# Optimization experiments

Measured on AMD Instinct MI355X. Metric: run time of the kernel, lower is better.

## Reference

```python
import jax, jax.numpy as jnp
import numpy as np


def _interp_bilinear_ac(x, out_h, out_w):
    """Bilinear resize with align_corners=True, NCHW."""
    n, c, h, w = x.shape
    ys = jnp.linspace(0.0, h - 1.0, out_h)
    xs = jnp.linspace(0.0, w - 1.0, out_w)
    y0 = jnp.floor(ys).astype(jnp.int32)
    y1 = jnp.minimum(y0 + 1, h - 1)
    wy = (ys - y0.astype(x.dtype))[None, None, :, None]
    x0 = jnp.floor(xs).astype(jnp.int32)
    x1 = jnp.minimum(x0 + 1, w - 1)
    wx = (xs - x0.astype(x.dtype))[None, None, None, :]
    # interpolate along H then W
    xh = x[:, :, y0, :] * (1.0 - wy) + x[:, :, y1, :] * wy  # [n,c,out_h,w]
    out = xh[:, :, :, x0] * (1.0 - wx) + xh[:, :, :, x1] * wx  # [n,c,out_h,out_w]
    return out


def setup_inputs() -> dict:
    key = jax.random.key(0)
    ks = jax.random.split(key, 7)
    return {
        "aspp": jax.random.normal(ks[0], (8, 128, 32, 32), jnp.float32),
        "f3": jax.random.normal(ks[1], (8, 128, 32, 32), jnp.float32),
        "inp": jax.random.normal(ks[2], (8, 4, 512, 512), jnp.float32),
        "cam": jax.random.normal(ks[3], (8, 21, 64, 64), jnp.float32),
        "w_aspp": jax.random.normal(ks[4], (64, 128), jnp.float32) * 0.05,
        "w_f3": jax.random.normal(ks[5], (64, 128), jnp.float32) * 0.05,
        "w_f9": jax.random.normal(ks[6], (128, 132), jnp.float32) * 0.05,
    }


def reference(aspp, f3, inp, cam, w_aspp, w_f3, w_f9):
    n, c, h, w = cam.shape
    # 1x1 convs (no bias) as channel matmuls
    f3p = jnp.einsum('oc,nchw->nohw', w_f3, f3)
    asppp = jnp.einsum('oc,nchw->nohw', w_aspp, aspp)
    # bilinear upsample (align_corners=True) to cam resolution
    asppp = _interp_bilinear_ac(asppp, h, w)
    x_s = _interp_bilinear_ac(inp, h, w)
    f3p = _interp_bilinear_ac(f3p, h, w)
    f = jnp.concatenate([x_s, asppp, f3p], axis=1)  # [n,132,h,w]
    f = jnp.einsum('oc,nchw->nohw', w_f9, f)        # [n,128,h,w]
    f = f.reshape(n, -1, h * w)                     # [n,128,hw]
    f = f / (jnp.linalg.norm(f, axis=1, keepdims=True) + 1e-5)
    # affinity: [n, hw, hw]
    aff = jax.nn.relu(jnp.einsum('ncp,ncq->npq', f, f))
    aff = aff / (jnp.sum(aff, axis=1, keepdims=True) + 1e-5)
    cam_rv = jnp.matmul(cam.reshape(n, -1, h * w), aff).reshape(n, -1, h, w)
    return cam_rv
```

## Files before the change

kernel.cpp:

```cpp
#include <hip/hip_runtime.h>
#include <math.h>

typedef unsigned short u16;
typedef unsigned int u32;
typedef __attribute__((ext_vector_type(8))) short bf16x8;
typedef __attribute__((ext_vector_type(4))) short short4v;
typedef __attribute__((ext_vector_type(4))) float f32x4;
typedef __attribute__((ext_vector_type(16))) float f32x16;

#define HW32 1024
#define HW64 4096
#define KCAM 21
#define PB 64
#define PSPLIT 4
#define FT_STR 168

static __device__ __forceinline__ u16 f2bf(float x) {
  u32 u = __float_as_uint(x);
  u32 r = (u + 0x7FFFu + ((u >> 16) & 1u)) >> 16;
  return (u16)r;
}
static __device__ __forceinline__ float bf2f(u16 h) {
  return __uint_as_float(((u32)h) << 16);
}

__global__ __launch_bounds__(256) void k_conv32(
    const float* __restrict__ aspp, const float* __restrict__ f3,
    const float* __restrict__ w_aspp, const float* __restrict__ w_f3,
    const float* __restrict__ w_f9,
    float* __restrict__ a32, float* __restrict__ g32,
    u16* __restrict__ whi, u16* __restrict__ wlo)
{
  const int pt = blockIdx.x, which = blockIdx.y >> 2, jq = blockIdx.y & 3,
            n = blockIdx.z;

  if (blockIdx.y == 0) {
    const int bid = blockIdx.z * 4 + blockIdx.x;
#pragma unroll
    for (int k = 0; k < 3; ++k) {
      const int idx = bid * 256 + threadIdx.x + k * 8192;
      if (idx < 128 * 160) {
        const int o = idx / 160, c = idx - o * 160;
        const float v = (c < 132) ? w_f9[o * 132 + c] : 0.f;
        const u16 h = f2bf(v);
        whi[idx] = h;
        wlo[idx] = f2bf(v - bf2f(h));
      }
    }
  }

  const float* x = (which == 0 ? aspp : f3) + (size_t)n * 128 * HW32;
  const float* w = (which == 0 ? w_aspp : w_f3) + jq * 16 * 128;
  float* out = (which == 0 ? a32 : g32) + (size_t)n * 64 * HW32 + (size_t)jq * 16 * HW32;

  __shared__ __align__(16) float wlds[16 * 128];
  for (int i = threadIdx.x; i < 16 * 128; i += 256) wlds[i] = w[i];
  __syncthreads();

  const int p = pt * 256 + threadIdx.x;
  float acc[16];
#pragma unroll
  for (int j = 0; j < 16; ++j) acc[j] = 0.f;

  for (int c0 = 0; c0 < 128; c0 += 8) {
    float xv[8];
#pragma unroll
    for (int cc = 0; cc < 8; ++cc) xv[cc] = x[(size_t)(c0 + cc) * HW32 + p];
#pragma unroll
    for (int j = 0; j < 16; ++j) {
      const float4 w0 = *reinterpret_cast<const float4*>(&wlds[j * 128 + c0]);
      const float4 w1 = *reinterpret_cast<const float4*>(&wlds[j * 128 + c0 + 4]);
      acc[j] = fmaf(w0.x, xv[0], acc[j]);
      acc[j] = fmaf(w0.y, xv[1], acc[j]);
      acc[j] = fmaf(w0.z, xv[2], acc[j]);
      acc[j] = fmaf(w0.w, xv[3], acc[j]);
      acc[j] = fmaf(w1.x, xv[4], acc[j]);
      acc[j] = fmaf(w1.y, xv[5], acc[j]);
      acc[j] = fmaf(w1.z, xv[6], acc[j]);
      acc[j] = fmaf(w1.w, xv[7], acc[j]);
    }
  }
  for (int j = 0; j < 16; ++j) out[(size_t)j * HW32 + p] = acc[j];
}

__global__ __launch_bounds__(256) void k_build_f(
    const float* __restrict__ inp, const float* __restrict__ a32,
    const float* __restrict__ g32, const u16* __restrict__ whi,
    const u16* __restrict__ wlo, const float* __restrict__ cam,
    u16* __restrict__ fhi_g, u16* __restrict__ camA)
{
  const int y2 = blockIdx.x, n = blockIdx.y;
  const int tid = threadIdx.x;

  __shared__ __align__(16) u16 feat[128 * FT_STR];
  __shared__ __align__(16) u16 wh[128 * FT_STR];
  __shared__ __align__(16) u16 wl[128 * FT_STR];

  for (int ch = tid; ch < 2560; ch += 256) {
    const int o = ch / 20, c8 = (ch - o * 20) * 8;
    *(bf16x8*)&wh[o * FT_STR + c8] = *(const bf16x8*)(whi + o * 160 + c8);
    *(bf16x8*)&wl[o * FT_STR + c8] = *(const bf16x8*)(wlo + o * 160 + c8);
  }

  {
    u16* dst = camA + ((size_t)n * 32 + y2) * HW64;
    if (y2 < KCAM) {
      const float* src = cam + ((size_t)n * KCAM + y2) * HW64;
      for (int i = tid; i < HW64; i += 256) dst[i] = f2bf(src[i]);
    } else {
      const u16 v = (y2 == KCAM) ? f2bf(1.f) : (u16)0;
      for (int i = tid; i < HW64; i += 256) dst[i] = v;
    }
  }

  const float s512 = 511.f / 63.f, s32 = 31.f / 63.f;
  const int yA0i = y2 * 2, yA1i = y2 * 2 + 1;
  const float sA0 = yA0i * s512, sA1 = yA1i * s512;
  const int y0A0 = (int)sA0, y0A1 = (int)sA1;
  const float wyA0 = sA0 - y0A0, wyA1 = sA1 - y0A1;
  const int y1A0 = min(y0A0 + 1, 511), y1A1 = min(y0A1 + 1, 511);
  const float sB0 = yA0i * s32, sB1 = yA1i * s32;
  const int y0B0 = (int)sB0, y0B1 = (int)sB1;
  const float wyB0 = sB0 - y0B0, wyB1 = sB1 - y0B1;
  const int y1B0 = min(y0B0 + 1, 31), y1B1 = min(y0B1 + 1, 31);

  for (int idx = tid; idx < 132 * 128; idx += 256) {
    const int c = idx >> 7;
    const int pos = idx & 127;
    const int ly = pos >> 6, x = pos & 63;
    const int y0A = ly ? y0A1 : y0A0, y1A = ly ? y1A1 : y1A0;
    const float wyA = ly ? wyA1 : wyA0;
    const int y0B = ly ? y0B1 : y0B0, y1B = ly ? y1B1 : y1B0;
    const float wyB = ly ? wyB1 : wyB0;
    float v;
    if (c < 4) {
      const float sx = x * s512;
      const int x0 = (int)sx;
      const float wx = sx - (float)x0;
      const int x1 = min(x0 + 1, 511);
      const float* im = inp + (size_t)(n * 4 + c) * 512 * 512;
      const float v00 = im[y0A * 512 + x0], v01 = im[y0A * 512 + x1];
      const float v10 = im[y1A * 512 + x0], v11 = im[y1A * 512 + x1];
      v = (v00 * (1.f - wx) + v01 * wx) * (1.f - wyA) +
          (v10 * (1.f - wx) + v11 * wx) * wyA;
    } else {
      const float* im = (c < 68) ? a32 + (size_t)(n * 64 + (c - 4)) * HW32
                                 : g32 + (size_t)(n * 64 + (c - 68)) * HW32;
      const float sx = x * s32;
      const int x0 = (int)sx;
      const float wx = sx - (float)x0;
      const int x1 = min(x0 + 1, 31);
      const float v00 = im[y0B * 32 + x0], v01 = im[y0B * 32 + x1];
      const float v10 = im[y1B * 32 + x0], v11 = im[y1B * 32 + x1];
      v = (v00 * (1.f - wx) + v01 * wx) * (1.f - wyB) +
          (v10 * (1.f - wx) + v11 * wx) * wyB;
    }
    feat[pos * FT_STR + c] = f2bf(v);
  }
  for (int idx = tid; idx < 28 * 128; idx += 256) {
    const int c = 132 + (idx >> 7), pos = idx & 127;
    feat[pos * FT_STR + c] = 0;
  }
  __syncthreads();

  const int lane = tid & 63, wave = tid >> 6;
  const int l15 = lane & 15, l4 = lane >> 4;

  f32x4 acc[8][2];
#pragma unroll
  for (int m = 0; m < 8; ++m)
#pragma unroll
    for (int nf = 0; nf < 2; ++nf) acc[m][nf] = {0.f, 0.f, 0.f, 0.f};

#pragma unroll
  for (int s = 0; s < 5; ++s) {
    bf16x8 B[2];
#pragma unroll
    for (int nf = 0; nf < 2; ++nf)
      B[nf] = *(const bf16x8*)&feat[(wave * 32 + nf * 16 + l15) * FT_STR +
                                    s * 32 + l4 * 8];
#pragma unroll
    for (int m = 0; m < 8; ++m) {
      const int wo = (m * 16 + l15) * FT_STR + s * 32 + l4 * 8;
      const bf16x8 Ahi = *(const bf16x8*)&wh[wo];
      const bf16x8 Alo = *(const bf16x8*)&wl[wo];
#pragma unroll
      for (int nf = 0; nf < 2; ++nf) {
        acc[m][nf] = __builtin_amdgcn_mfma_f32_16x16x32_bf16(Ahi, B[nf], acc[m][nf], 0, 0, 0);
        acc[m][nf] = __builtin_amdgcn_mfma_f32_16x16x32_bf16(Alo, B[nf], acc[m][nf], 0, 0, 0);
      }
    }
  }

#pragma unroll
  for (int nf = 0; nf < 2; ++nf) {
    float ss = 0.f;
#pragma unroll
    for (int m = 0; m < 8; ++m)
#pragma unroll
      for (int i = 0; i < 4; ++i) ss = fmaf(acc[m][nf][i], acc[m][nf][i], ss);
    ss += __shfl_xor(ss, 16);
    ss += __shfl_xor(ss, 32);
    const float inv = 1.f / (sqrtf(ss) + 1e-5f);
    const int pos = wave * 32 + nf * 16 + l15;
    u16* fp = fhi_g + ((size_t)n * HW64 + (size_t)(y2 * 2 + (pos >> 6)) * 64 +
                       (pos & 63)) * 128 + l4 * 4;
#pragma unroll
    for (int m = 0; m < 8; ++m) {
      const float v0 = acc[m][nf][0] * inv, v1 = acc[m][nf][1] * inv;
      const float v2 = acc[m][nf][2] * inv, v3 = acc[m][nf][3] * inv;
      union { u32 d[2]; short4v h; } P;
      asm("v_cvt_pk_bf16_f32 %0, %1, %2" : "=v"(P.d[0]) : "v"(v0), "v"(v1));
      asm("v_cvt_pk_bf16_f32 %0, %1, %2" : "=v"(P.d[1]) : "v"(v2), "v"(v3));
      *(short4v*)(fp + m * 16) = P.h;
    }
  }
}

__global__ __launch_bounds__(256) void k_fused(
    const u16* __restrict__ fhi_g, const u16* __restrict__ camA,
    float* __restrict__ part)
{
  __shared__ __align__(16) u16 fh[2][PB * 128];

  const int gx = blockIdx.x;
  const int n = gx & 7;
  const int rest = gx >> 3;
  const int qt = rest & 15;
  const int ps = rest >> 4;
  const int tid = threadIdx.x;
  const int lane = tid & 63;
  const int wq = tid >> 6;
  const int l31 = lane & 31;
  const int lh = lane >> 5;
  const int qb = qt * 256;

  const u16* fbase = fhi_g + (size_t)n * HW64 * 128;

  bf16x8 Bq[2][8];
#pragma unroll
  for (int qh = 0; qh < 2; ++qh) {
    const size_t rowo = (size_t)(qb + wq * 64 + qh * 32 + l31) * 128;
#pragma unroll
    for (int ks = 0; ks < 8; ++ks)
      Bq[qh][ks] = *(const bf16x8*)(fbase + rowo + ks * 16 + lh * 8);
  }

  f32x16 nacc0, nacc1;
#pragma unroll
  for (int i = 0; i < 16; ++i) { nacc0[i] = 0.f; nacc1[i] = 0.f; }

  const int p_base = ps * (HW64 / PSPLIT);
  const int sp = tid >> 2;
  const int scb = (tid & 3) * 64;
  const int xorw = (sp & 7) << 4;
  int wofs[4];
#pragma unroll
  for (int k = 0; k < 4; ++k)
    wofs[k] = sp * 128 + (((scb + k * 16) ^ xorw) >> 1);
  const int xorr = (l31 & 7) << 4;

  {
    const u16* src = fbase + (size_t)(p_base + sp) * 128 + scb / 2;
#pragma unroll
    for (int k = 0; k < 4; ++k)
      *(bf16x8*)&fh[0][wofs[k]] = *(const bf16x8*)(src + k * 8);
  }

  int cur = 0;
  for (int t = 0; t < (HW64 / PSPLIT) / PB; ++t) {
    const int p0 = p_base + t * PB;
    __syncthreads();

    bf16x8 nxt[4];
    if (t < 15) {
      const u16* src = fbase + (size_t)(p0 + PB + sp) * 128 + scb / 2;
#pragma unroll
      for (int k = 0; k < 4; ++k) nxt[k] = *(const bf16x8*)(src + k * 8);
    }

    bf16x8 Ac[4];
#pragma unroll
    for (int kst = 0; kst < 4; ++kst) {
      union { short4v h[2]; bf16x8 v; } A;
      const u16* cp = camA + ((size_t)n * 32 + l31) * HW64 + p0 + kst * 16 + lh * 4;
      A.h[0] = *(const short4v*)cp;
      A.h[1] = *(const short4v*)(cp + 8);
      Ac[kst] = A.v;
    }

    f32x16 accS[2][2];
#pragma unroll
    for (int ks = 0; ks < 8; ++ks) {
      const int cb = (ks * 32 + (lh << 4)) ^ xorr;
      bf16x8 Ah[2];
#pragma unroll
      for (int mt = 0; mt < 2; ++mt)
        Ah[mt] = *(const bf16x8*)&fh[cur][(mt * 32 + l31) * 128 + (cb >> 1)];
      if (ks == 0) {
        f32x16 z;
#pragma unroll
        for (int i = 0; i < 16; ++i) z[i] = 0.f;
#pragma unroll
        for (int mt = 0; mt < 2; ++mt) {
          accS[mt][0] = __builtin_amdgcn_mfma_f32_32x32x16_bf16(Ah[mt], Bq[0][0], z, 0, 0, 0);
          accS[mt][1] = __builtin_amdgcn_mfma_f32_32x32x16_bf16(Ah[mt], Bq[1][0], z, 0, 0, 0);
        }
      } else {
#pragma unroll
        for (int mt = 0; mt < 2; ++mt) {
          accS[mt][0] = __builtin_amdgcn_mfma_f32_32x32x16_bf16(Ah[mt], Bq[0][ks], accS[mt][0], 0, 0, 0);
          accS[mt][1] = __builtin_amdgcn_mfma_f32_32x32x16_bf16(Ah[mt], Bq[1][ks], accS[mt][1], 0, 0, 0);
        }
      }
    }

#pragma unroll
    for (int kst = 0; kst < 4; ++kst) {
      const int mt = kst >> 1, h8 = (kst & 1) * 8;
#pragma unroll
      for (int qh = 0; qh < 2; ++qh) {
        union { u32 d[4]; bf16x8 v; } W;
#pragma unroll
        for (int i = 0; i < 4; ++i) {
          const float a0 = fmaxf(accS[mt][qh][h8 + 2 * i], 0.f);
          const float a1 = fmaxf(accS[mt][qh][h8 + 2 * i + 1], 0.f);
          asm("v_cvt_pk_bf16_f32 %0, %1, %2" : "=v"(W.d[i]) : "v"(a0), "v"(a1));
        }
        if (qh == 0)
          nacc0 = __builtin_amdgcn_mfma_f32_32x32x16_bf16(Ac[kst], W.v, nacc0, 0, 0, 0);
        else
          nacc1 = __builtin_amdgcn_mfma_f32_32x32x16_bf16(Ac[kst], W.v, nacc1, 0, 0, 0);
      }
    }

    if (t < 15) {
#pragma unroll
      for (int k = 0; k < 4; ++k) *(bf16x8*)&fh[cur ^ 1][wofs[k]] = nxt[k];
    }
    cur ^= 1;
  }

#pragma unroll
  for (int qh = 0; qh < 2; ++qh) {
    const int qg = qb + wq * 64 + qh * 32 + l31;
#pragma unroll
    for (int r = 0; r < 16; ++r) {
      const int row = (r & 3) + 8 * (r >> 2) + 4 * lh;
      if (row < 22)
        part[(((size_t)n * PSPLIT + ps) * 22 + row) * HW64 + qg] =
            (qh == 0) ? nacc0[r] : nacc1[r];
    }
  }
}

__global__ __launch_bounds__(256) void k_final(
    const float* __restrict__ part, float* __restrict__ out, int total)
{
  const int idx = blockIdx.x * 256 + threadIdx.x;
  if (idx >= total) return;
  const int n = idx / (KCAM * HW64);
  const int r = idx - n * (KCAM * HW64);
  const int k = r >> 12;
  const int q = r & 4095;
  const float* base = part + (size_t)n * PSPLIT * 22 * HW64;
  float num = 0.f, den = 0.f;
#pragma unroll
  for (int p = 0; p < PSPLIT; ++p) {
    num += base[((size_t)p * 22 + k) * HW64 + q];
    den += base[((size_t)p * 22 + 21) * HW64 + q];
  }
  out[idx] = num / (den + 1e-5f);
}

extern "C" void kernel_launch(void* const* d_in, const int* in_sizes, int n_in,
                              void* d_out, int out_size, void* d_ws, size_t ws_size,
                              hipStream_t stream) {
  const float* aspp   = (const float*)d_in[0];
  const float* f3     = (const float*)d_in[1];
  const float* inp    = (const float*)d_in[2];
  const float* cam    = (const float*)d_in[3];
  const float* w_aspp = (const float*)d_in[4];
  const float* w_f3   = (const float*)d_in[5];
  const float* w_f9   = (const float*)d_in[6];
  float* out = (float*)d_out;

  u16*   fhi  = (u16*)d_ws;
  u16*   camA = fhi + 4194304;
  u16*   whi  = camA + 1048576;
  u16*   wlo  = whi + 20480;
  float* part = (float*)(wlo + 20480);
  float* a32  = part;
  float* g32  = a32 + 524288;

  k_conv32<<<dim3(4, 8, 8), 256, 0, stream>>>(aspp, f3, w_aspp, w_f3, w_f9,
                                              a32, g32, whi, wlo);
  k_build_f<<<dim3(32, 8), 256, 0, stream>>>(inp, a32, g32, whi, wlo, cam,
                                             fhi, camA);
  k_fused<<<512, 256, 0, stream>>>(fhi, camA, part);
  k_final<<<2688, 256, 0, stream>>>(part, out, 8 * KCAM * HW64);
}
```

Baseline: 99.61 us.

## Fuse split-K reduction into main kernel via last-block atomic counter

Removes the separate k_final launch. Each k_fused block increments a per-(n,qt) counter after writing its partial sums, and the last of the PSPLIT blocks to arrive reduces the partials and writes the normalized output. This saves one kernel launch and its scheduling gap. In exchange it adds a memset launch, threadfences, and a serialized tail in which only the last block per tile does the reduction.

After: 186.8 us. 1.88x slower.

```diff
diff --git a/kernel.cpp b/kernel.cpp
--- a/kernel.cpp
+++ b/kernel.cpp
@@ -219,9 +219,10 @@
 
 __global__ __launch_bounds__(256) void k_fused(
     const u16* __restrict__ fhi_g, const u16* __restrict__ camA,
-    float* __restrict__ part)
+    float* __restrict__ part, float* __restrict__ out, int* __restrict__ cnt)
 {
   __shared__ __align__(16) u16 fh[2][PB * 128];
+  __shared__ int lastFlag;
 
   const int gx = blockIdx.x;
   const int n = gx & 7;
@@ -352,25 +353,27 @@
             (qh == 0) ? nacc0[r] : nacc1[r];
     }
   }
-}
-
-__global__ __launch_bounds__(256) void k_final(
-    const float* __restrict__ part, float* __restrict__ out, int total)
-{
-  const int idx = blockIdx.x * 256 + threadIdx.x;
-  if (idx >= total) return;
-  const int n = idx / (KCAM * HW64);
-  const int r = idx - n * (KCAM * HW64);
-  const int k = r >> 12;
-  const int q = r & 4095;
-  const float* base = part + (size_t)n * PSPLIT * 22 * HW64;
-  float num = 0.f, den = 0.f;
-#pragma unroll
-  for (int p = 0; p < PSPLIT; ++p) {
-    num += base[((size_t)p * 22 + k) * HW64 + q];
-    den += base[((size_t)p * 22 + 21) * HW64 + q];
-  }
-  out[idx] = num / (den + 1e-5f);
+
+  __threadfence();
+  __syncthreads();
+  if (tid == 0)
+    lastFlag = (atomicAdd(&cnt[n * 16 + qt], 1) == PSPLIT - 1);
+  __syncthreads();
+  if (lastFlag) {
+    __threadfence();
+    const int q = qb + tid;
+    const float* pb = part + (size_t)n * PSPLIT * 22 * HW64 + q;
+    float den = 0.f;
+#pragma unroll
+    for (int p = 0; p < PSPLIT; ++p) den += pb[((size_t)p * 22 + 21) * HW64];
+    const float inv = 1.f / (den + 1e-5f);
+    for (int row = 0; row < KCAM; ++row) {
+      float num = 0.f;
+#pragma unroll
+      for (int p = 0; p < PSPLIT; ++p) num += pb[((size_t)p * 22 + row) * HW64];
+      out[((size_t)n * KCAM + row) * HW64 + q] = num * inv;
+    }
+  }
 }
 
 extern "C" void kernel_launch(void* const* d_in, const int* in_sizes, int n_in,
@@ -390,13 +393,14 @@
   u16*   whi  = camA + 1048576;
   u16*   wlo  = whi + 20480;
   float* part = (float*)(wlo + 20480);
+  int*   cnt  = (int*)(part + 2883584);
   float* a32  = part;
   float* g32  = a32 + 524288;
 
+  hipMemsetAsync(cnt, 0, 128 * sizeof(int), stream);
   k_conv32<<<dim3(4, 8, 8), 256, 0, stream>>>(aspp, f3, w_aspp, w_f3, w_f9,
                                               a32, g32, whi, wlo);
   k_build_f<<<dim3(32, 8), 256, 0, stream>>>(inp, a32, g32, whi, wlo, cam,
                                              fhi, camA);
-  k_fused<<<512, 256, 0, stream>>>(fhi, camA, part);
-  k_final<<<2688, 256, 0, stream>>>(part, out, 8 * KCAM * HW64);
-}
+  k_fused<<<512, 256, 0, stream>>>(fhi, camA, part, out, cnt);
+}
```

## Software-pipeline affinity stages by deferring second MFMA stage one tile

Applied to the files above, without the earlier changes.

The fused affinity/cam kernel loop is unrolled by two, and the second-stage MFMA (cam times relu'd affinity tile) for a tile now runs after the first-stage MFMAs of the next tile. Ping-pong register buffers hold the packed weights and cam fragments. The goal is to hide the dependency between stage-1 accumulators, the relu/bf16 pack, and stage-2 MFMAs by interleaving independent work. The cost is higher register pressure from the extra W and Ac buffers, which could lower occupancy or cause spills.

Measured after the change: 106.0 us. 6.4% more time.

```diff
diff --git a/kernel.cpp b/kernel.cpp
--- a/kernel.cpp
+++ b/kernel.cpp
@@ -217,6 +217,62 @@
   }
 }
 
+#define STAGE1_M(ACC)                                                          \
+  _Pragma("unroll")                                                            \
+  for (int ks = 0; ks < 8; ++ks) {                                             \
+    const int cb = (ks * 32 + (lh << 4)) ^ xorr;                               \
+    bf16x8 Ah0 = *(const bf16x8*)&fh[cur][(l31) * 128 + (cb >> 1)];            \
+    bf16x8 Ah1 = *(const bf16x8*)&fh[cur][(32 + l31) * 128 + (cb >> 1)];       \
+    if (ks == 0) {                                                             \
+      f32x16 z;                                                                \
+      _Pragma("unroll") for (int i = 0; i < 16; ++i) z[i] = 0.f;               \
+      ACC[0][0] = __builtin_amdgcn_mfma_f32_32x32x16_bf16(Ah0, Bq[0][0], z, 0, 0, 0); \
+      ACC[0][1] = __builtin_amdgcn_mfma_f32_32x32x16_bf16(Ah0, Bq[1][0], z, 0, 0, 0); \
+      ACC[1][0] = __builtin_amdgcn_mfma_f32_32x32x16_bf16(Ah1, Bq[0][0], z, 0, 0, 0); \
+      ACC[1][1] = __builtin_amdgcn_mfma_f32_32x32x16_bf16(Ah1, Bq[1][0], z, 0, 0, 0); \
+    } else {                                                                   \
+      ACC[0][0] = __builtin_amdgcn_mfma_f32_32x32x16_bf16(Ah0, Bq[0][ks], ACC[0][0], 0, 0, 0); \
+      ACC[0][1] = __builtin_amdgcn_mfma_f32_32x32x16_bf16(Ah0, Bq[1][ks], ACC[0][1], 0, 0, 0); \
+      ACC[1][0] = __builtin_amdgcn_mfma_f32_32x32x16_bf16(Ah1, Bq[0][ks], ACC[1][0], 0, 0, 0); \
+      ACC[1][1] = __builtin_amdgcn_mfma_f32_32x32x16_bf16(Ah1, Bq[1][ks], ACC[1][1], 0, 0, 0); \
+    }                                                                          \
+  }
+
+#define PACK_M(ACC, W)                                                         \
+  _Pragma("unroll")                                                            \
+  for (int kst = 0; kst < 4; ++kst) {                                          \
+    const int mt = kst >> 1, h8 = (kst & 1) * 8;                               \
+    _Pragma("unroll")                                                          \
+    for (int qh = 0; qh < 2; ++qh) {                                           \
+      _Pragma("unroll")                                                        \
+      for (int i = 0; i < 4; ++i) {                                            \
+        const float a0 = fmaxf(ACC[mt][qh][h8 + 2 * i], 0.f);                  \
+        const float a1 = fmaxf(ACC[mt][qh][h8 + 2 * i + 1], 0.f);              \
+        asm("v_cvt_pk_bf16_f32 %0, %1, %2" : "=v"(W[kst][qh][i]) : "v"(a0), "v"(a1)); \
+      }                                                                        \
+    }                                                                          \
+  }
+
+#define MFMA2_M(W, AC)                                                         \
+  _Pragma("unroll")                                                            \
+  for (int kst = 0; kst < 4; ++kst) {                                          \
+    union { u32 d[4]; bf16x8 v; } W0, W1;                                      \
+    _Pragma("unroll")                                                          \
+    for (int i = 0; i < 4; ++i) { W0.d[i] = W[kst][0][i]; W1.d[i] = W[kst][1][i]; } \
+    nacc0 = __builtin_amdgcn_mfma_f32_32x32x16_bf16(AC[kst], W0.v, nacc0, 0, 0, 0); \
+    nacc1 = __builtin_amdgcn_mfma_f32_32x32x16_bf16(AC[kst], W1.v, nacc1, 0, 0, 0); \
+  }
+
+#define LOADAC_M(AC, P0)                                                       \
+  _Pragma("unroll")                                                            \
+  for (int kst = 0; kst < 4; ++kst) {                                          \
+    union { short4v h[2]; bf16x8 v; } A;                                       \
+    const u16* cp = camA + ((size_t)n * 32 + l31) * HW64 + (P0) + kst * 16 + lh * 4; \
+    A.h[0] = *(const short4v*)cp;                                              \
+    A.h[1] = *(const short4v*)(cp + 8);                                        \
+    AC[kst] = A.v;                                                             \
+  }
+
 __global__ __launch_bounds__(256) void k_fused(
     const u16* __restrict__ fhi_g, const u16* __restrict__ camA,
     float* __restrict__ part)
@@ -267,79 +323,51 @@
       *(bf16x8*)&fh[0][wofs[k]] = *(const bf16x8*)(src + k * 8);
   }
 
+  u32 WA[4][2][4], WB[4][2][4];
+  bf16x8 AcA[4], AcB[4];
   int cur = 0;
-  for (int t = 0; t < (HW64 / PSPLIT) / PB; ++t) {
-    const int p0 = p_base + t * PB;
-    __syncthreads();
-
-    bf16x8 nxt[4];
-    if (t < 15) {
-      const u16* src = fbase + (size_t)(p0 + PB + sp) * 128 + scb / 2;
-#pragma unroll
-      for (int k = 0; k < 4; ++k) nxt[k] = *(const bf16x8*)(src + k * 8);
-    }
-
-    bf16x8 Ac[4];
-#pragma unroll
-    for (int kst = 0; kst < 4; ++kst) {
-      union { short4v h[2]; bf16x8 v; } A;
-      const u16* cp = camA + ((size_t)n * 32 + l31) * HW64 + p0 + kst * 16 + lh * 4;
-      A.h[0] = *(const short4v*)cp;
-      A.h[1] = *(const short4v*)(cp + 8);
-      Ac[kst] = A.v;
-    }
-
-    f32x16 accS[2][2];
-#pragma unroll
-    for (int ks = 0; ks < 8; ++ks) {
-      const int cb = (ks * 32 + (lh << 4)) ^ xorr;
-      bf16x8 Ah[2];
-#pragma unroll
-      for (int mt = 0; mt < 2; ++mt)
-        Ah[mt] = *(const bf16x8*)&fh[cur][(mt * 32 + l31) * 128 + (cb >> 1)];
-      if (ks == 0) {
-        f32x16 z;
-#pragma unroll
-        for (int i = 0; i < 16; ++i) z[i] = 0.f;
-#pragma unroll
-        for (int mt = 0; mt < 2; ++mt) {
-          accS[mt][0] = __builtin_amdgcn_mfma_f32_32x32x16_bf16(Ah[mt], Bq[0][0], z, 0, 0, 0);
-          accS[mt][1] = __builtin_amdgcn_mfma_f32_32x32x16_bf16(Ah[mt], Bq[1][0], z, 0, 0, 0);
-        }
-      } else {
-#pragma unroll
-        for (int mt = 0; mt < 2; ++mt) {
-          accS[mt][0] = __builtin_amdgcn_mfma_f32_32x32x16_bf16(Ah[mt], Bq[0][ks], accS[mt][0], 0, 0, 0);
-          accS[mt][1] = __builtin_amdgcn_mfma_f32_32x32x16_bf16(Ah[mt], Bq[1][ks], accS[mt][1], 0, 0, 0);
-        }
+
+  for (int tt = 0; tt < 8; ++tt) {
+    {
+      const int p0 = p_base + (2 * tt) * PB;
+      __syncthreads();
+      bf16x8 nxt[4];
+      {
+        const u16* src = fbase + (size_t)(p0 + PB + sp) * 128 + scb / 2;
+#pragma unroll
+        for (int k = 0; k < 4; ++k) nxt[k] = *(const bf16x8*)(src + k * 8);
       }
-    }
-
-#pragma unroll
-    for (int kst = 0; kst < 4; ++kst) {
-      const int mt = kst >> 1, h8 = (kst & 1) * 8;
-#pragma unroll
-      for (int qh = 0; qh < 2; ++qh) {
-        union { u32 d[4]; bf16x8 v; } W;
-#pragma unroll
-        for (int i = 0; i < 4; ++i) {
-          const float a0 = fmaxf(accS[mt][qh][h8 + 2 * i], 0.f);
-          const float a1 = fmaxf(accS[mt][qh][h8 + 2 * i + 1], 0.f);
-          asm("v_cvt_pk_bf16_f32 %0, %1, %2" : "=v"(W.d[i]) : "v"(a0), "v"(a1));
-        }
-        if (qh == 0)
-          nacc0 = __builtin_amdgcn_mfma_f32_32x32x16_bf16(Ac[kst], W.v, nacc0, 0, 0, 0);
-        else
-          nacc1 = __builtin_amdgcn_mfma_f32_32x32x16_bf16(Ac[kst], W.v, nacc1, 0, 0, 0);
+      LOADAC_M(AcA, p0)
+      f32x16 accS[2][2];
+      STAGE1_M(accS)
+      if (tt > 0) { MFMA2_M(WB, AcB) }
+      PACK_M(accS, WA)
+#pragma unroll
+      for (int k = 0; k < 4; ++k) *(bf16x8*)&fh[cur ^ 1][wofs[k]] = nxt[k];
+      cur ^= 1;
+    }
+    {
+      const int p0 = p_base + (2 * tt + 1) * PB;
+      __syncthreads();
+      bf16x8 nxt[4];
+      if (tt < 7) {
+        const u16* src = fbase + (size_t)(p0 + PB + sp) * 128 + scb / 2;
+#pragma unroll
+        for (int k = 0; k < 4; ++k) nxt[k] = *(const bf16x8*)(src + k * 8);
       }
-    }
-
-    if (t < 15) {
-#pragma unroll
-      for (int k = 0; k < 4; ++k) *(bf16x8*)&fh[cur ^ 1][wofs[k]] = nxt[k];
-    }
-    cur ^= 1;
-  }
+      LOADAC_M(AcB, p0)
+      f32x16 accS[2][2];
+      STAGE1_M(accS)
+      MFMA2_M(WA, AcA)
+      PACK_M(accS, WB)
+      if (tt < 7) {
+#pragma unroll
+        for (int k = 0; k < 4; ++k) *(bf16x8*)&fh[cur ^ 1][wofs[k]] = nxt[k];
+      }
+      cur ^= 1;
+    }
+  }
+  MFMA2_M(WB, AcB)
 
 #pragma unroll
   for (int qh = 0; qh < 2; ++qh) {
```

## Fold 1x1 aspp/f3 convs into w_f9 weights and upsample raw inputs

Applied to the files above, without the earlier changes.

Since bilinear interpolation and 1x1 convolution are both linear, the aspp and f3 projections are folded into the final w_f9 matrix by a small weight-prep kernel. The per-pixel conv32 pass and its intermediate buffers go away. k_build_f now interpolates the raw 128-channel aspp and f3 maps directly and runs two K-chunks of MFMA against the combined weights. This removes one kernel and its global round trip, but build_f now does more interpolation and twice the MFMA work, and the combined weights are quantised to a bf16 hi/lo split.

Measured after the change: 134.9 us. +35.4%, slower.

```diff
diff --git a/kernel.cpp b/kernel.cpp
--- a/kernel.cpp
+++ b/kernel.cpp
@@ -24,69 +24,41 @@
   return __uint_as_float(((u32)h) << 16);
 }
 
-__global__ __launch_bounds__(256) void k_conv32(
-    const float* __restrict__ aspp, const float* __restrict__ f3,
+__global__ __launch_bounds__(256) void k_prep(
     const float* __restrict__ w_aspp, const float* __restrict__ w_f3,
     const float* __restrict__ w_f9,
-    float* __restrict__ a32, float* __restrict__ g32,
-    u16* __restrict__ whi, u16* __restrict__ wlo)
+    u16* __restrict__ wch, u16* __restrict__ wcl)
 {
-  const int pt = blockIdx.x, which = blockIdx.y >> 2, jq = blockIdx.y & 3,
-            n = blockIdx.z;
-
-  if (blockIdx.y == 0) {
-    const int bid = blockIdx.z * 4 + blockIdx.x;
-#pragma unroll
-    for (int k = 0; k < 3; ++k) {
-      const int idx = bid * 256 + threadIdx.x + k * 8192;
-      if (idx < 128 * 160) {
-        const int o = idx / 160, c = idx - o * 160;
-        const float v = (c < 132) ? w_f9[o * 132 + c] : 0.f;
-        const u16 h = f2bf(v);
-        whi[idx] = h;
-        wlo[idx] = f2bf(v - bf2f(h));
-      }
-    }
-  }
-
-  const float* x = (which == 0 ? aspp : f3) + (size_t)n * 128 * HW32;
-  const float* w = (which == 0 ? w_aspp : w_f3) + jq * 16 * 128;
-  float* out = (which == 0 ? a32 : g32) + (size_t)n * 64 * HW32 + (size_t)jq * 16 * HW32;
-
-  __shared__ __align__(16) float wlds[16 * 128];
-  for (int i = threadIdx.x; i < 16 * 128; i += 256) wlds[i] = w[i];
-  __syncthreads();
-
-  const int p = pt * 256 + threadIdx.x;
-  float acc[16];
-#pragma unroll
-  for (int j = 0; j < 16; ++j) acc[j] = 0.f;
-
-  for (int c0 = 0; c0 < 128; c0 += 8) {
-    float xv[8];
-#pragma unroll
-    for (int cc = 0; cc < 8; ++cc) xv[cc] = x[(size_t)(c0 + cc) * HW32 + p];
-#pragma unroll
-    for (int j = 0; j < 16; ++j) {
-      const float4 w0 = *reinterpret_cast<const float4*>(&wlds[j * 128 + c0]);
-      const float4 w1 = *reinterpret_cast<const float4*>(&wlds[j * 128 + c0 + 4]);
-      acc[j] = fmaf(w0.x, xv[0], acc[j]);
-      acc[j] = fmaf(w0.y, xv[1], acc[j]);
-      acc[j] = fmaf(w0.z, xv[2], acc[j]);
-      acc[j] = fmaf(w0.w, xv[3], acc[j]);
-      acc[j] = fmaf(w1.x, xv[4], acc[j]);
-      acc[j] = fmaf(w1.y, xv[5], acc[j]);
-      acc[j] = fmaf(w1.z, xv[6], acc[j]);
-      acc[j] = fmaf(w1.w, xv[7], acc[j]);
-    }
-  }
-  for (int j = 0; j < 16; ++j) out[(size_t)j * HW32 + p] = acc[j];
+  const int ob = blockIdx.x * 8;
+  for (int e = threadIdx.x; e < 8 * 320; e += 256) {
+    const int o = ob + (e / 320);
+    const int kk = e % 320;
+    const int chunk = kk / 160, k = kk - chunk * 160;
+    float v = 0.f;
+    if (chunk == 0) {
+      if (k < 4) {
+        v = w_f9[o * 132 + k];
+      } else if (k < 132) {
+        const int j = k - 4;
+        for (int u = 0; u < 64; ++u)
+          v = fmaf(w_f9[o * 132 + 4 + u], w_aspp[u * 128 + j], v);
+      }
+    } else {
+      if (k < 128) {
+        for (int u = 0; u < 64; ++u)
+          v = fmaf(w_f9[o * 132 + 68 + u], w_f3[u * 128 + k], v);
+      }
+    }
+    const u16 h = f2bf(v);
+    wch[(chunk * 128 + o) * 160 + k] = h;
+    wcl[(chunk * 128 + o) * 160 + k] = f2bf(v - bf2f(h));
+  }
 }
 
 __global__ __launch_bounds__(256) void k_build_f(
-    const float* __restrict__ inp, const float* __restrict__ a32,
-    const float* __restrict__ g32, const u16* __restrict__ whi,
-    const u16* __restrict__ wlo, const float* __restrict__ cam,
+    const float* __restrict__ inp, const float* __restrict__ aspp,
+    const float* __restrict__ f3g, const u16* __restrict__ wch,
+    const u16* __restrict__ wcl, const float* __restrict__ cam,
     u16* __restrict__ fhi_g, u16* __restrict__ camA)
 {
   const int y2 = blockIdx.x, n = blockIdx.y;
@@ -95,12 +67,6 @@
   __shared__ __align__(16) u16 feat[128 * FT_STR];
   __shared__ __align__(16) u16 wh[128 * FT_STR];
   __shared__ __align__(16) u16 wl[128 * FT_STR];
-
-  for (int ch = tid; ch < 2560; ch += 256) {
-    const int o = ch / 20, c8 = (ch - o * 20) * 8;
-    *(bf16x8*)&wh[o * FT_STR + c8] = *(const bf16x8*)(whi + o * 160 + c8);
-    *(bf16x8*)&wl[o * FT_STR + c8] = *(const bf16x8*)(wlo + o * 160 + c8);
-  }
 
   {
     u16* dst = camA + ((size_t)n * 32 + y2) * HW64;
@@ -124,45 +90,6 @@
   const float wyB0 = sB0 - y0B0, wyB1 = sB1 - y0B1;
   const int y1B0 = min(y0B0 + 1, 31), y1B1 = min(y0B1 + 1, 31);
 
-  for (int idx = tid; idx < 132 * 128; idx += 256) {
-    const int c = idx >> 7;
-    const int pos = idx & 127;
-    const int ly = pos >> 6, x = pos & 63;
-    const int y0A = ly ? y0A1 : y0A0, y1A = ly ? y1A1 : y1A0;
-    const float wyA = ly ? wyA1 : wyA0;
-    const int y0B = ly ? y0B1 : y0B0, y1B = ly ? y1B1 : y1B0;
-    const float wyB = ly ? wyB1 : wyB0;
-    float v;
-    if (c < 4) {
-      const float sx = x * s512;
-      const int x0 = (int)sx;
-      const float wx = sx - (float)x0;
-      const int x1 = min(x0 + 1, 511);
-      const float* im = inp + (size_t)(n * 4 + c) * 512 * 512;
-      const float v00 = im[y0A * 512 + x0], v01 = im[y0A * 512 + x1];
-      const float v10 = im[y1A * 512 + x0], v11 = im[y1A * 512 + x1];
-      v = (v00 * (1.f - wx) + v01 * wx) * (1.f - wyA) +
-          (v10 * (1.f - wx) + v11 * wx) * wyA;
-    } else {
-      const float* im = (c < 68) ? a32 + (size_t)(n * 64 + (c - 4)) * HW32
-                                 : g32 + (size_t)(n * 64 + (c - 68)) * HW32;
-      const float sx = x * s32;
-      const int x0 = (int)sx;
-      const float wx = sx - (float)x0;
-      const int x1 = min(x0 + 1, 31);
-      const float v00 = im[y0B * 32 + x0], v01 = im[y0B * 32 + x1];
-      const float v10 = im[y1B * 32 + x0], v11 = im[y1B * 32 + x1];
-      v = (v00 * (1.f - wx) + v01 * wx) * (1.f - wyB) +
-          (v10 * (1.f - wx) + v11 * wx) * wyB;
-    }
-    feat[pos * FT_STR + c] = f2bf(v);
-  }
-  for (int idx = tid; idx < 28 * 128; idx += 256) {
-    const int c = 132 + (idx >> 7), pos = idx & 127;
-    feat[pos * FT_STR + c] = 0;
-  }
-  __syncthreads();
-
   const int lane = tid & 63, wave = tid >> 6;
   const int l15 = lane & 15, l4 = lane >> 4;
 
@@ -173,23 +100,84 @@
     for (int nf = 0; nf < 2; ++nf) acc[m][nf] = {0.f, 0.f, 0.f, 0.f};
 
 #pragma unroll
-  for (int s = 0; s < 5; ++s) {
-    bf16x8 B[2];
-#pragma unroll
-    for (int nf = 0; nf < 2; ++nf)
-      B[nf] = *(const bf16x8*)&feat[(wave * 32 + nf * 16 + l15) * FT_STR +
-                                    s * 32 + l4 * 8];
-#pragma unroll
-    for (int m = 0; m < 8; ++m) {
-      const int wo = (m * 16 + l15) * FT_STR + s * 32 + l4 * 8;
-      const bf16x8 Ahi = *(const bf16x8*)&wh[wo];
-      const bf16x8 Alo = *(const bf16x8*)&wl[wo];
-#pragma unroll
-      for (int nf = 0; nf < 2; ++nf) {
-        acc[m][nf] = __builtin_amdgcn_mfma_f32_16x16x32_bf16(Ahi, B[nf], acc[m][nf], 0, 0, 0);
-        acc[m][nf] = __builtin_amdgcn_mfma_f32_16x16x32_bf16(Alo, B[nf], acc[m][nf], 0, 0, 0);
-      }
-    }
+  for (int chunk = 0; chunk < 2; ++chunk) {
+    for (int ch = tid; ch < 2560; ch += 256) {
+      const int o = ch / 20, c8 = (ch - o * 20) * 8;
+      const int go = (chunk * 128 + o) * 160 + c8;
+      *(bf16x8*)&wh[o * FT_STR + c8] = *(const bf16x8*)(wch + go);
+      *(bf16x8*)&wl[o * FT_STR + c8] = *(const bf16x8*)(wcl + go);
+    }
+
+    for (int idx = tid; idx < 160 * 128; idx += 256) {
+      const int c = idx >> 7;
+      const int pos = idx & 127;
+      const int ly = pos >> 6, x = pos & 63;
+      float v = 0.f;
+      if (chunk == 0) {
+        if (c < 4) {
+          const int y0A = ly ? y0A1 : y0A0, y1A = ly ? y1A1 : y1A0;
+          const float wyA = ly ? wyA1 : wyA0;
+          const float sx = x * s512;
+          const int x0 = (int)sx;
+          const float wx = sx - (float)x0;
+          const int x1 = min(x0 + 1, 511);
+          const float* im = inp + (size_t)(n * 4 + c) * 512 * 512;
+          const float v00 = im[y0A * 512 + x0], v01 = im[y0A * 512 + x1];
+          const float v10 = im[y1A * 512 + x0], v11 = im[y1A * 512 + x1];
+          v = (v00 * (1.f - wx) + v01 * wx) * (1.f - wyA) +
+              (v10 * (1.f - wx) + v11 * wx) * wyA;
+        } else if (c < 132) {
+          const int y0B = ly ? y0B1 : y0B0, y1B = ly ? y1B1 : y1B0;
+          const float wyB = ly ? wyB1 : wyB0;
+          const float* im = aspp + ((size_t)n * 128 + (c - 4)) * HW32;
+          const float sx = x * s32;
+          const int x0 = (int)sx;
+          const float wx = sx - (float)x0;
+          const int x1 = min(x0 + 1, 31);
+          const float v00 = im[y0B * 32 + x0], v01 = im[y0B * 32 + x1];
+          const float v10 = im[y1B * 32 + x0], v11 = im[y1B * 32 + x1];
+          v = (v00 * (1.f - wx) + v01 * wx) * (1.f - wyB) +
+              (v10 * (1.f - wx) + v11 * wx) * wyB;
+        }
+      } else {
+        if (c < 128) {
+          const int y0B = ly ? y0B1 : y0B0, y1B = ly ? y1B1 : y1B0;
+          const float wyB = ly ? wyB1 : wyB0;
+          const float* im = f3g + ((size_t)n * 128 + c) * HW32;
+          const float sx = x * s32;
+          const int x0 = (int)sx;
+          const float wx = sx - (float)x0;
+          const int x1 = min(x0 + 1, 31);
+          const float v00 = im[y0B * 32 + x0], v01 = im[y0B * 32 + x1];
+          const float v10 = im[y1B * 32 + x0], v11 = im[y1B * 32 + x1];
+          v = (v00 * (1.f - wx) + v01 * wx) * (1.f - wyB) +
+              (v10 * (1.f - wx) + v11 * wx) * wyB;
+        }
+      }
+      feat[pos * FT_STR + c] = f2bf(v);
+    }
+    __syncthreads();
+
+#pragma unroll
+    for (int s = 0; s < 5; ++s) {
+      bf16x8 B[2];
+#pragma unroll
+      for (int nf = 0; nf < 2; ++nf)
+        B[nf] = *(const bf16x8*)&feat[(wave * 32 + nf * 16 + l15) * FT_STR +
+                                      s * 32 + l4 * 8];
+#pragma unroll
+      for (int m = 0; m < 8; ++m) {
+        const int wo = (m * 16 + l15) * FT_STR + s * 32 + l4 * 8;
+        const bf16x8 Ahi = *(const bf16x8*)&wh[wo];
+        const bf16x8 Alo = *(const bf16x8*)&wl[wo];
+#pragma unroll
+        for (int nf = 0; nf < 2; ++nf) {
+          acc[m][nf] = __builtin_amdgcn_mfma_f32_16x16x32_bf16(Ahi, B[nf], acc[m][nf], 0, 0, 0);
+          acc[m][nf] = __builtin_amdgcn_mfma_f32_16x16x32_bf16(Alo, B[nf], acc[m][nf], 0, 0, 0);
+        }
+      }
+    }
+    __syncthreads();
   }
 
 #pragma unroll
@@ -387,15 +375,12 @@
 
   u16*   fhi  = (u16*)d_ws;
   u16*   camA = fhi + 4194304;
-  u16*   whi  = camA + 1048576;
-  u16*   wlo  = whi + 20480;
-  float* part = (float*)(wlo + 20480);
-  float* a32  = part;
-  float* g32  = a32 + 524288;
-
-  k_conv32<<<dim3(4, 8, 8), 256, 0, stream>>>(aspp, f3, w_aspp, w_f3, w_f9,
-                                              a32, g32, whi, wlo);
-  k_build_f<<<dim3(32, 8), 256, 0, stream>>>(inp, a32, g32, whi, wlo, cam,
+  u16*   wch  = camA + 1048576;
+  u16*   wcl  = wch + 40960;
+  float* part = (float*)(wcl + 40960);
+
+  k_prep<<<16, 256, 0, stream>>>(w_aspp, w_f3, w_f9, wch, wcl);
+  k_build_f<<<dim3(32, 8), 256, 0, stream>>>(inp, aspp, f3, wch, wcl, cam,
                                              fhi, camA);
   k_fused<<<512, 256, 0, stream>>>(fhi, camA, part);
   k_final<<<2688, 256, 0, stream>>>(part, out, 8 * KCAM * HW64);
```
